# Kernel tuning notes

Measured on AMD Instinct MI355X. Metric: run time of the kernel, lower is better.

Reference implementation:

```python
import jax, jax.numpy as jnp
import numpy as np

N = 50000      # nodes
E = 600000     # edges
D_IN = 7       # input feature dim (Attn_head(7,128))
H = 128        # hidden dim
L = 2          # n_layer - 1 iterations actually executed


def _attn_head(x, edge_index, W, a1, a2, b, Wres):
    # GAT head over edge_index: h=xW; logit_e = leakyrelu(a1.h[src] + a2.h[dst]);
    # per-destination segment softmax; scatter-add aggregate; bias+residual+SELU.
    n = x.shape[0]
    h = x @ W                              # [N,H]
    src, dst = edge_index[0], edge_index[1]
    f1 = h @ a1                            # [N]
    f2 = h @ a2                            # [N]
    logits = jax.nn.leaky_relu(f1[src] + f2[dst], 0.2)   # [E]
    m = jax.ops.segment_max(logits, dst, num_segments=n)
    e = jnp.exp(logits - m[dst])
    s = jax.ops.segment_sum(e, dst, num_segments=n)
    coef = e / (s[dst] + 1e-9)             # [E] softmax over incoming edges
    out = jax.ops.segment_sum(coef[:, None] * h[src], dst, num_segments=n) + b
    res = x @ Wres if Wres is not None else x
    return jax.nn.selu(out + res)


def _simple_att(x3, Wa, ba, ua):
    # HAN-style attention pooling over axis 1. x3: [N,T,H]
    v = jnp.tanh(x3 @ Wa + ba)             # [N,T,H]
    vu = jnp.einsum('nth,h->nt', v, ua)    # [N,T]
    alphas = jax.nn.softmax(vu, axis=1)
    return jnp.einsum('nth,nt->nh', x3, alphas)  # [N,H]


def setup_inputs() -> dict:
    key = jax.random.key(0)
    ks = jax.random.split(key, 20)
    def rn(k, shape, s=0.1):
        return jax.random.normal(k, shape, dtype=jnp.float32) * s
    inp = {
        'x': jax.random.normal(ks[0], (N, D_IN), dtype=jnp.float32),
        'edge_index': jax.random.randint(ks[1], (2, E), 0, N, dtype=jnp.int64),
        # input GAT head (7 -> 128) with residual projection
        'W0': rn(ks[2], (D_IN, H)), 'a1_0': rn(ks[3], (H,)), 'a2_0': rn(ks[4], (H,)),
        'b0': jnp.zeros((H,), jnp.float32), 'Wr0': rn(ks[5], (D_IN, H)),
        # initial SimpleAttLayer
        'Wa0': rn(ks[6], (H, H)), 'ba0': jnp.zeros((H,), jnp.float32), 'ua0': rn(ks[7], (H,)),
        # L stacked final GAT heads (128 -> 128, identity residual)
        'Wf': rn(ks[8], (L, H, H)), 'a1f': rn(ks[9], (L, H)), 'a2f': rn(ks[10], (L, H)),
        'bf': jnp.zeros((L, H), jnp.float32),
        # L final SimpleAttLayers
        'Waf': rn(ks[11], (L, H, H)), 'baf': jnp.zeros((L, H), jnp.float32), 'uaf': rn(ks[12], (L, H)),
        # fc 128 -> 1
        'Wfc': rn(ks[13], (H, 1)), 'bfc': jnp.zeros((1,), jnp.float32),
    }
    return inp


def reference(x, edge_index, W0, a1_0, a2_0, b0, Wr0, Wa0, ba0, ua0,
              Wf, a1f, a2f, bf, Waf, baf, uaf, Wfc, bfc):
    h = _attn_head(x, edge_index, W0, a1_0, a2_0, b0, Wr0)       # [N,H]
    final = _simple_att(h[:, None, :], Wa0, ba0, ua0)            # [N,H]
    for i in range(L):
        lo = _attn_head(final, edge_index, Wf[i], a1f[i], a2f[i], bf[i], None)
        lo = _simple_att(lo[:, None, :], Waf[i], baf[i], uaf[i])
        final = final + lo
    y = final[-1] @ Wfc + bfc                                    # last node -> [1]
    return jax.nn.leaky_relu(y, 0.01)
```

## Files before the change

kernel.cpp:

```cpp
#include <hip/hip_runtime.h>
#include <hip/hip_bf16.h>

#define C0   8192
#define C1   2048
#define CE1  32768
#define CE2  2048

struct KP {
  const float* x; const int* ei;
  const float* W0; const float* a1_0; const float* a2_0; const float* b0; const float* Wr0;
  const float* Wf; const float* a1f; const float* a2f; const float* bf;
  const float* Wfc; const float* bfc;
  float* out;
  int N, E, t;
  int* cnt;
  float* wa;
  int* idx0; int* idx1; int* list0; int* list1;
  float* s0; float* acc0; float* s1; float* acc1;
  int* e1s; int* e1d; int* e2s;
  float* f0; float* hh0; float* av10; float* av20;
  float* f1; float* hh1; float* av11; float* av21;
};

__device__ __forceinline__ float lrelu(float v, float a){ return v >= 0.f ? v : a*v; }
__device__ __forceinline__ float selu_f(float v){
  const float sc = 1.0507009873554805f, al = 1.6732632423543772f;
  return v > 0.f ? sc*v : sc*al*expm1f(v);
}
__device__ __forceinline__ void claim(int* idx, int* list, int* cnt, int cap, int node,
                                      float* s, float* acc){
  if (atomicCAS(&idx[node], -1, -2) == -1){
    int slot = atomicAdd(cnt, 1);
    if (slot < cap){
      list[slot] = node;
      s[slot] = 0.f;
      float4* a = (float4*)(acc + (size_t)slot * 128);
      #pragma unroll
      for (int k = 0; k < 32; ++k) a[k] = make_float4(0.f,0.f,0.f,0.f);
      idx[node] = slot;
    }
  }
}

__global__ void k_init(KP p){
  int u = blockIdx.x*blockDim.x + threadIdx.x;
  if (u < p.N){
    int v = (u == p.t) ? 0 : -1;
    p.idx0[u] = v; p.idx1[u] = v;
  }
  if (blockIdx.x == 0){
    int tid = threadIdx.x;
    if (tid < 7){
      float sA = 0.f, sB = 0.f;
      for (int k = 0; k < 128; ++k){ float wv = p.W0[tid*128+k]; sA += wv*p.a1_0[k]; sB += wv*p.a2_0[k]; }
      p.wa[tid] = sA; p.wa[8+tid] = sB;
    }
    if (tid < 128){ p.acc0[tid] = 0.f; p.acc1[tid] = 0.f; }
    else if (tid == 128){
      p.s0[0] = 0.f; p.s1[0] = 0.f; p.list0[0] = p.t; p.list1[0] = p.t;
      p.cnt[1] = 0; p.cnt[2] = 0; p.cnt[3] = 1; p.cnt[4] = 1;
    }
  }
}

__global__ void k_scan1(KP p){
  int gtid = blockIdx.x*blockDim.x + threadIdx.x;
  int nv = p.E >> 2;
  const int4* d4 = (const int4*)(p.ei + p.E);
  if (gtid < nv){
    int4 dv = d4[gtid];
    #pragma unroll
    for (int m = 0; m < 4; ++m){
      int dd = (&dv.x)[m];
      if (dd == p.t){
        int s = p.ei[4*gtid + m];
        int slot = atomicAdd(&p.cnt[2], 1);
        if (slot < CE2) p.e2s[slot] = s;
        claim(p.idx1, p.list1, &p.cnt[4], C1, s, p.s1, p.acc1);
        claim(p.idx0, p.list0, &p.cnt[3], C0, s, p.s0, p.acc0);
      }
    }
  }
  if (gtid < (p.E & 3)){
    int i = nv*4 + gtid;
    int dd = p.ei[p.E + i];
    if (dd == p.t){
      int s = p.ei[i];
      int slot = atomicAdd(&p.cnt[2], 1);
      if (slot < CE2) p.e2s[slot] = s;
      claim(p.idx1, p.list1, &p.cnt[4], C1, s, p.s1, p.acc1);
      claim(p.idx0, p.list0, &p.cnt[3], C0, s, p.s0, p.acc0);
    }
  }
}

__global__ void k_scan2(KP p){
  __shared__ int bm[2048];
  int tid = threadIdx.x;
  int bmw = (p.N + 31) >> 5;
  for (int i = tid; i < bmw; i += blockDim.x) bm[i] = 0;
  __syncthreads();
  int n1 = min(p.cnt[4], C1);
  for (int i = tid; i < n1; i += blockDim.x){ int u = p.list1[i]; atomicOr(&bm[u>>5], 1 << (u&31)); }
  __syncthreads();
  int gtid = blockIdx.x*blockDim.x + tid;
  int nv = p.E >> 2;
  const int4* d4 = (const int4*)(p.ei + p.E);
  if (gtid < nv){
    int4 dv = d4[gtid];
    #pragma unroll
    for (int m = 0; m < 4; ++m){
      int dd = (&dv.x)[m];
      if ((bm[dd>>5] >> (dd&31)) & 1){
        int s = p.ei[4*gtid + m];
        int slot = atomicAdd(&p.cnt[1], 1);
        if (slot < CE1){ p.e1s[slot] = s; p.e1d[slot] = dd; }
        claim(p.idx0, p.list0, &p.cnt[3], C0, s, p.s0, p.acc0);
      }
    }
  }
  if (gtid < (p.E & 3)){
    int i = nv*4 + gtid;
    int dd = p.ei[p.E + i];
    if ((bm[dd>>5] >> (dd&31)) & 1){
      int s = p.ei[i];
      int slot = atomicAdd(&p.cnt[1], 1);
      if (slot < CE1){ p.e1s[slot] = s; p.e1d[slot] = dd; }
      claim(p.idx0, p.list0, &p.cnt[3], C0, s, p.s0, p.acc0);
    }
  }
}

__global__ void k_scan3(KP p){
  __shared__ int bm[2048];
  int tid = threadIdx.x;
  int bmw = (p.N + 31) >> 5;
  for (int i = tid; i < bmw; i += blockDim.x) bm[i] = 0;
  __syncthreads();
  int n0 = min(p.cnt[3], C0);
  for (int i = tid; i < n0; i += blockDim.x){ int u = p.list0[i]; atomicOr(&bm[u>>5], 1 << (u&31)); }
  __syncthreads();
  int gtid = blockIdx.x*blockDim.x + tid;
  int lane = tid & 63;
  int nv = p.E >> 2;
  const int4* d4 = (const int4*)(p.ei + p.E);
  bool inb = gtid < nv;
  int4 dv = make_int4(-1,-1,-1,-1);
  if (inb) dv = d4[gtid];
  #pragma unroll
  for (int m = 0; m < 4; ++m){
    int dd = inb ? (&dv.x)[m] : -1;
    bool match = (dd >= 0) && ((bm[dd>>5] >> (dd&31)) & 1);
    int sv = 0;
    if (match) sv = p.ei[4*gtid + m];
    unsigned long long b = __ballot(match);
    while (b){
      int l = __ffsll((long long)b) - 1; b &= b - 1;
      int s = __shfl(sv, l), d = __shfl(dd, l);
      float f = 0.f;
      #pragma unroll
      for (int j = 0; j < 7; ++j) f += p.x[s*7+j]*p.wa[j] + p.x[d*7+j]*p.wa[8+j];
      float e = expf(lrelu(f, 0.2f));
      int id = p.idx0[d];
      if (id >= 0){
        float h0 = 0.f, h1 = 0.f;
        #pragma unroll
        for (int j = 0; j < 7; ++j){
          float xs = p.x[s*7+j];
          float2 w2 = *(const float2*)&p.W0[j*128 + 2*lane];
          h0 += xs*w2.x; h1 += xs*w2.y;
        }
        atomicAdd(&p.acc0[(size_t)id*128 + 2*lane    ], e*h0);
        atomicAdd(&p.acc0[(size_t)id*128 + 2*lane + 1], e*h1);
        if (lane == 0) atomicAdd(&p.s0[id], e);
      }
    }
  }
  if (gtid < (p.E & 3)){
    int i = nv*4 + gtid;
    int dd = p.ei[p.E + i];
    if ((bm[dd>>5] >> (dd&31)) & 1){
      int s = p.ei[i];
      float f = 0.f;
      for (int j = 0; j < 7; ++j) f += p.x[s*7+j]*p.wa[j] + p.x[dd*7+j]*p.wa[8+j];
      float e = expf(lrelu(f, 0.2f));
      int id = p.idx0[dd];
      if (id >= 0){
        for (int k = 0; k < 128; ++k){
          float h = 0.f;
          for (int j = 0; j < 7; ++j) h += p.x[s*7+j]*p.W0[j*128+k];
          atomicAdd(&p.acc0[(size_t)id*128 + k], e*h);
        }
        atomicAdd(&p.s0[id], e);
      }
    }
  }
}

__global__ void __launch_bounds__(128) k_fin0(KP p){
  __shared__ float sf[128];
  __shared__ float2 red[128];
  int tid = threadIdx.x;
  int n0 = min(p.cnt[3], C0);
  for (int b = blockIdx.x; b < n0; b += gridDim.x){
    int u = p.list0[b];
    float res = 0.f;
    #pragma unroll
    for (int j = 0; j < 7; ++j) res += p.x[u*7+j]*p.Wr0[j*128+tid];
    float v = selu_f(p.acc0[(size_t)b*128+tid]/(p.s0[b]+1e-9f) + p.b0[tid] + res);
    p.f0[(size_t)b*128+tid] = v;
    sf[tid] = v;
    __syncthreads();
    float hv = 0.f;
    #pragma unroll 8
    for (int j = 0; j < 128; ++j) hv += sf[j]*p.Wf[j*128+tid];
    p.hh0[(size_t)b*128+tid] = hv;
    red[tid] = make_float2(hv*p.a1f[tid], hv*p.a2f[tid]);
    __syncthreads();
    for (int st = 64; st > 0; st >>= 1){
      if (tid < st){ red[tid].x += red[tid+st].x; red[tid].y += red[tid+st].y; }
      __syncthreads();
    }
    if (tid == 0){ p.av10[b] = red[0].x; p.av20[b] = red[0].y; }
    __syncthreads();
  }
}

__global__ void k_agg1(KP p){
  int gtid = blockIdx.x*blockDim.x + threadIdx.x;
  int wv = gtid >> 6, lane = gtid & 63;
  int nw = (gridDim.x*blockDim.x) >> 6;
  int ne1 = min(p.cnt[1], CE1);
  for (int i = wv; i < ne1; i += nw){
    int s = p.e1s[i], d = p.e1d[i];
    int i0s = p.idx0[s], i0d = p.idx0[d], i1 = p.idx1[d];
    if (i0s < 0 || i1 < 0) continue;
    float e = expf(lrelu(p.av10[i0s] + p.av20[i0d], 0.2f));
    float2 hv = *(const float2*)&p.hh0[(size_t)i0s*128 + 2*lane];
    atomicAdd(&p.acc1[(size_t)i1*128 + 2*lane    ], e*hv.x);
    atomicAdd(&p.acc1[(size_t)i1*128 + 2*lane + 1], e*hv.y);
    if (lane == 0) atomicAdd(&p.s1[i1], e);
  }
}

__global__ void __launch_bounds__(128) k_fin1(KP p){
  __shared__ float sf[128];
  __shared__ float2 red[128];
  int tid = threadIdx.x;
  int n1 = min(p.cnt[4], C1);
  for (int b = blockIdx.x; b < n1; b += gridDim.x){
    int u = p.list1[b];
    int i0 = p.idx0[u];
    float f0v = (i0 >= 0) ? p.f0[(size_t)i0*128+tid] : 0.f;
    float lo = selu_f(p.acc1[(size_t)b*128+tid]/(p.s1[b]+1e-9f) + p.bf[tid] + f0v);
    float v = f0v + lo;
    p.f1[(size_t)b*128+tid] = v;
    sf[tid] = v;
    __syncthreads();
    float hv = 0.f;
    #pragma unroll 8
    for (int j = 0; j < 128; ++j) hv += sf[j]*p.Wf[16384 + j*128+tid];
    p.hh1[(size_t)b*128+tid] = hv;
    red[tid] = make_float2(hv*p.a1f[128+tid], hv*p.a2f[128+tid]);
    __syncthreads();
    for (int st = 64; st > 0; st >>= 1){
      if (tid < st){ red[tid].x += red[tid+st].x; red[tid].y += red[tid+st].y; }
      __syncthreads();
    }
    if (tid == 0){ p.av11[b] = red[0].x; p.av21[b] = red[0].y; }
    __syncthreads();
  }
}

__global__ void __launch_bounds__(128) k_l2(KP p){
  __shared__ float se[128];
  __shared__ int   si[128];
  __shared__ float red[128];
  int tid = threadIdx.x;
  int ne2 = min(p.cnt[2], CE2);
  float acc = 0.f, s2 = 0.f;
  for (int base = 0; base < ne2; base += 128){
    int i = base + tid;
    float e = 0.f; int ii = -1;
    if (i < ne2){
      ii = p.idx1[p.e2s[i]];
      if (ii >= 0) e = expf(lrelu(p.av11[ii] + p.av21[0], 0.2f));
    }
    se[tid] = e; si[tid] = ii;
    __syncthreads();
    int c = min(128, ne2 - base);
    for (int q = 0; q < c; ++q){
      if (si[q] >= 0){
        s2  += se[q];
        acc += se[q]*p.hh1[(size_t)si[q]*128 + tid];
      }
    }
    __syncthreads();
  }
  float f1v = p.f1[tid];
  float lo = selu_f(acc/(s2+1e-9f) + p.bf[128+tid] + f1v);
  red[tid] = (f1v + lo)*p.Wfc[tid];
  __syncthreads();
  for (int st = 64; st > 0; st >>= 1){ if (tid < st) red[tid] += red[tid+st]; __syncthreads(); }
  if (tid == 0) p.out[0] = lrelu(red[0] + p.bfc[0], 0.01f);
}

extern "C" void kernel_launch(void* const* d_in, const int* in_sizes, int n_in,
                              void* d_out, int out_size, void* d_ws, size_t ws_size,
                              hipStream_t stream){
  (void)n_in; (void)out_size;
  KP p;
  p.x    = (const float*)d_in[0];
  p.ei   = (const int*)  d_in[1];
  p.W0   = (const float*)d_in[2];
  p.a1_0 = (const float*)d_in[3];
  p.a2_0 = (const float*)d_in[4];
  p.b0   = (const float*)d_in[5];
  p.Wr0  = (const float*)d_in[6];
  p.Wf   = (const float*)d_in[10];
  p.a1f  = (const float*)d_in[11];
  p.a2f  = (const float*)d_in[12];
  p.bf   = (const float*)d_in[13];
  p.Wfc  = (const float*)d_in[17];
  p.bfc  = (const float*)d_in[18];
  p.out  = (float*)d_out;

  p.N = in_sizes[0] / 7;
  p.E = in_sizes[1] / 2;
  p.t = p.N - 1;

  char* q = (char*)d_ws;
  auto alloc = [&](size_t bytes) -> void* {
    void* r = (void*)q;
    q += (bytes + 255) & ~(size_t)255;
    return r;
  };
  p.cnt  = (int*)  alloc(64);
  p.wa   = (float*)alloc(sizeof(float)*16);
  p.idx0 = (int*)  alloc(sizeof(int)*(size_t)p.N);
  p.idx1 = (int*)  alloc(sizeof(int)*(size_t)p.N);
  p.list0= (int*)  alloc(sizeof(int)*C0);
  p.list1= (int*)  alloc(sizeof(int)*C1);
  p.s0   = (float*)alloc(sizeof(float)*C0);
  p.acc0 = (float*)alloc(sizeof(float)*(size_t)C0*128);
  p.s1   = (float*)alloc(sizeof(float)*C1);
  p.acc1 = (float*)alloc(sizeof(float)*(size_t)C1*128);
  p.e1s  = (int*)  alloc(sizeof(int)*CE1);
  p.e1d  = (int*)  alloc(sizeof(int)*CE1);
  p.e2s  = (int*)  alloc(sizeof(int)*CE2);
  p.f0   = (float*)alloc(sizeof(float)*(size_t)C0*128);
  p.hh0  = (float*)alloc(sizeof(float)*(size_t)C0*128);
  p.av10 = (float*)alloc(sizeof(float)*C0);
  p.av20 = (float*)alloc(sizeof(float)*C0);
  p.f1   = (float*)alloc(sizeof(float)*(size_t)C1*128);
  p.hh1  = (float*)alloc(sizeof(float)*(size_t)C1*128);
  p.av11 = (float*)alloc(sizeof(float)*C1);
  p.av21 = (float*)alloc(sizeof(float)*C1);
  if ((size_t)(q - (char*)d_ws) > ws_size) return;

  int nb  = (p.N + 255) / 256;
  int eb4 = ((p.E >> 2) + 255) / 256;
  k_init <<<nb , 256, 0, stream>>>(p);
  k_scan1<<<eb4, 256, 0, stream>>>(p);
  k_scan2<<<eb4, 256, 0, stream>>>(p);
  k_scan3<<<eb4, 256, 0, stream>>>(p);
  k_fin0 <<<256, 128, 0, stream>>>(p);
  k_agg1 <<<64 , 256, 0, stream>>>(p);
  k_fin1 <<<32 , 128, 0, stream>>>(p);
  k_l2   <<<1  , 128, 0, stream>>>(p);
}
```

Before: 49.03 us.

## Fuse layer-1 aggregation, finalize and last-node layer into one single-block kernel

```diff
diff --git a/kernel.cpp b/kernel.cpp
--- a/kernel.cpp
+++ b/kernel.cpp
@@ -5,6 +5,7 @@
 #define C1   2048
 #define CE1  32768
 #define CE2  2048
+#define FT   1024
 
 struct KP {
   const float* x; const int* ei;
@@ -226,83 +227,111 @@
   }
 }
 
-__global__ void k_agg1(KP p){
-  int gtid = blockIdx.x*blockDim.x + threadIdx.x;
-  int wv = gtid >> 6, lane = gtid & 63;
-  int nw = (gridDim.x*blockDim.x) >> 6;
+__global__ void __launch_bounds__(FT) k_final(KP p){
+  __shared__ float ev[FT];
+  __shared__ int   eis[FT];
+  __shared__ int   ei1[FT];
+  __shared__ float sfx[8][128];
+  __shared__ float2 rd[8][128];
+  __shared__ float se2[128];
+  __shared__ int   si2[128];
+  __shared__ float redl[128];
+  int tid = threadIdx.x;
+
   int ne1 = min(p.cnt[1], CE1);
-  for (int i = wv; i < ne1; i += nw){
-    int s = p.e1s[i], d = p.e1d[i];
-    int i0s = p.idx0[s], i0d = p.idx0[d], i1 = p.idx1[d];
-    if (i0s < 0 || i1 < 0) continue;
-    float e = expf(lrelu(p.av10[i0s] + p.av20[i0d], 0.2f));
-    float2 hv = *(const float2*)&p.hh0[(size_t)i0s*128 + 2*lane];
-    atomicAdd(&p.acc1[(size_t)i1*128 + 2*lane    ], e*hv.x);
-    atomicAdd(&p.acc1[(size_t)i1*128 + 2*lane + 1], e*hv.y);
-    if (lane == 0) atomicAdd(&p.s1[i1], e);
-  }
-}
-
-__global__ void __launch_bounds__(128) k_fin1(KP p){
-  __shared__ float sf[128];
-  __shared__ float2 red[128];
-  int tid = threadIdx.x;
+  for (int base = 0; base < ne1; base += FT){
+    int i = base + tid;
+    float e = 0.f; int i0s = -1, i1 = -1;
+    if (i < ne1){
+      int s = p.e1s[i], d = p.e1d[i];
+      i0s = p.idx0[s]; int i0d = p.idx0[d]; i1 = p.idx1[d];
+      if (i0s >= 0 && i1 >= 0){
+        e = expf(lrelu(p.av10[i0s] + p.av20[i0d], 0.2f));
+        atomicAdd(&p.s1[i1], e);
+      } else i0s = -1;
+    }
+    ev[tid] = e; eis[tid] = i0s; ei1[tid] = i1;
+    __syncthreads();
+    int c = min(FT, ne1 - base);
+    int total = c << 7;
+    for (int idx = tid; idx < total; idx += FT){
+      int ee = idx >> 7, ch = idx & 127;
+      int s0i = eis[ee];
+      if (s0i >= 0)
+        atomicAdd(&p.acc1[(size_t)ei1[ee]*128 + ch], ev[ee]*p.hh0[(size_t)s0i*128 + ch]);
+    }
+    __syncthreads();
+  }
+
   int n1 = min(p.cnt[4], C1);
-  for (int b = blockIdx.x; b < n1; b += gridDim.x){
-    int u = p.list1[b];
-    int i0 = p.idx0[u];
-    float f0v = (i0 >= 0) ? p.f0[(size_t)i0*128+tid] : 0.f;
-    float lo = selu_f(p.acc1[(size_t)b*128+tid]/(p.s1[b]+1e-9f) + p.bf[tid] + f0v);
-    float v = f0v + lo;
-    p.f1[(size_t)b*128+tid] = v;
-    sf[tid] = v;
-    __syncthreads();
-    float hv = 0.f;
-    #pragma unroll 8
-    for (int j = 0; j < 128; ++j) hv += sf[j]*p.Wf[16384 + j*128+tid];
-    p.hh1[(size_t)b*128+tid] = hv;
-    red[tid] = make_float2(hv*p.a1f[128+tid], hv*p.a2f[128+tid]);
+  int bq = tid >> 7, ch = tid & 127;
+  for (int base = 0; base < n1; base += 8){
+    int b = base + bq;
+    bool act = (b < n1);
+    if (act){
+      int u = p.list1[b];
+      int i0 = p.idx0[u];
+      float f0v = (i0 >= 0) ? p.f0[(size_t)i0*128 + ch] : 0.f;
+      float lo = selu_f(p.acc1[(size_t)b*128 + ch]/(p.s1[b] + 1e-9f) + p.bf[ch] + f0v);
+      float v = f0v + lo;
+      p.f1[(size_t)b*128 + ch] = v;
+      sfx[bq][ch] = v;
+    }
+    __syncthreads();
+    if (act){
+      float hv = 0.f;
+      #pragma unroll 8
+      for (int j = 0; j < 128; ++j) hv += sfx[bq][j]*p.Wf[16384 + j*128 + ch];
+      p.hh1[(size_t)b*128 + ch] = hv;
+      rd[bq][ch] = make_float2(hv*p.a1f[128+ch], hv*p.a2f[128+ch]);
+    }
     __syncthreads();
     for (int st = 64; st > 0; st >>= 1){
-      if (tid < st){ red[tid].x += red[tid+st].x; red[tid].y += red[tid+st].y; }
+      if (act && ch < st){
+        rd[bq][ch].x += rd[bq][ch+st].x;
+        rd[bq][ch].y += rd[bq][ch+st].y;
+      }
       __syncthreads();
     }
-    if (tid == 0){ p.av11[b] = red[0].x; p.av21[b] = red[0].y; }
-    __syncthreads();
-  }
-}
-
-__global__ void __launch_bounds__(128) k_l2(KP p){
-  __shared__ float se[128];
-  __shared__ int   si[128];
-  __shared__ float red[128];
-  int tid = threadIdx.x;
+    if (act && ch == 0){ p.av11[b] = rd[bq][0].x; p.av21[b] = rd[bq][0].y; }
+    __syncthreads();
+  }
+
   int ne2 = min(p.cnt[2], CE2);
-  float acc = 0.f, s2 = 0.f;
+  float acc = 0.f, ssum = 0.f;
   for (int base = 0; base < ne2; base += 128){
     int i = base + tid;
-    float e = 0.f; int ii = -1;
-    if (i < ne2){
-      ii = p.idx1[p.e2s[i]];
-      if (ii >= 0) e = expf(lrelu(p.av11[ii] + p.av21[0], 0.2f));
-    }
-    se[tid] = e; si[tid] = ii;
-    __syncthreads();
-    int c = min(128, ne2 - base);
-    for (int q = 0; q < c; ++q){
-      if (si[q] >= 0){
-        s2  += se[q];
-        acc += se[q]*p.hh1[(size_t)si[q]*128 + tid];
-      }
-    }
-    __syncthreads();
-  }
-  float f1v = p.f1[tid];
-  float lo = selu_f(acc/(s2+1e-9f) + p.bf[128+tid] + f1v);
-  red[tid] = (f1v + lo)*p.Wfc[tid];
-  __syncthreads();
-  for (int st = 64; st > 0; st >>= 1){ if (tid < st) red[tid] += red[tid+st]; __syncthreads(); }
-  if (tid == 0) p.out[0] = lrelu(red[0] + p.bfc[0], 0.01f);
+    if (tid < 128){
+      float e = 0.f; int ii = -1;
+      if (i < ne2){
+        ii = p.idx1[p.e2s[i]];
+        if (ii >= 0) e = expf(lrelu(p.av11[ii] + p.av21[0], 0.2f));
+      }
+      se2[tid] = e; si2[tid] = ii;
+    }
+    __syncthreads();
+    if (tid < 128){
+      int c = min(128, ne2 - base);
+      for (int q = 0; q < c; ++q){
+        if (si2[q] >= 0){
+          ssum += se2[q];
+          acc  += se2[q]*p.hh1[(size_t)si2[q]*128 + tid];
+        }
+      }
+    }
+    __syncthreads();
+  }
+  if (tid < 128){
+    float f1v = p.f1[tid];
+    float lo = selu_f(acc/(ssum + 1e-9f) + p.bf[128+tid] + f1v);
+    redl[tid] = (f1v + lo)*p.Wfc[tid];
+  }
+  __syncthreads();
+  for (int st = 64; st > 0; st >>= 1){
+    if (tid < st) redl[tid] += redl[tid+st];
+    __syncthreads();
+  }
+  if (tid == 0) p.out[0] = lrelu(redl[0] + p.bfc[0], 0.01f);
 }
 
 extern "C" void kernel_launch(void* const* d_in, const int* in_sizes, int n_in,
@@ -365,7 +394,5 @@
   k_scan2<<<eb4, 256, 0, stream>>>(p);
   k_scan3<<<eb4, 256, 0, stream>>>(p);
   k_fin0 <<<256, 128, 0, stream>>>(p);
-  k_agg1 <<<64 , 256, 0, stream>>>(p);
-  k_fin1 <<<32 , 128, 0, stream>>>(p);
-  k_l2   <<<1  , 128, 0, stream>>>(p);
-}
+  k_final<<<1  , FT , 0, stream>>>(p);
+}
```

New measurement: 57.71 us. 1.18x slower.
